# Kernel optimization log

Measured on AMD Instinct MI355X. Metric: run time of the kernel, lower is better.

Reference implementation:

```python
import jax, jax.numpy as jnp
import numpy as np

IN_BW = 4
W_BW = 4
EPS = 1e-5


def quantize(x, bw):
    # k-bit uniform quantizer on [-1, 1 - 2^(1-bw)] with straight-through rounding
    scale = 2.0 ** (bw - 1)
    xc = jnp.clip(x, -1.0, 1.0 - 1.0 / scale)
    q = jnp.round(xc * scale) / scale
    return xc + jax.lax.stop_gradient(q - xc)


def bconv(x, w, stride):
    # BinarizeConv2d: quantize activations (in_bw) and weights (weight_bw), then conv
    return jax.lax.conv_general_dilated(
        quantize(x, IN_BW), quantize(w, W_BW),
        window_strides=stride, padding='VALID',
        dimension_numbers=('NCHW', 'OIHW', 'NCHW'))


def bn2d(x, g, b):
    mean = x.mean(axis=(0, 2, 3), keepdims=True)
    var = x.var(axis=(0, 2, 3), keepdims=True)
    return (x - mean) * jax.lax.rsqrt(var + EPS) * g.reshape(1, -1, 1, 1) + b.reshape(1, -1, 1, 1)


def bn1d(x, g, b):
    mean = x.mean(axis=0, keepdims=True)
    var = x.var(axis=0, keepdims=True)
    return (x - mean) * jax.lax.rsqrt(var + EPS) * g + b


def htanh(x):
    return jnp.clip(x, -1.0, 1.0)


def setup_inputs() -> dict:
    key = jax.random.key(0)
    ks = jax.random.split(key, 24)
    B = 8192
    d = {'x': jax.random.normal(ks[0], (B, 1, 1250, 1), dtype=jnp.float32)}
    # conv weights OIHW
    shapes = [(3, 1, 6, 1), (5, 3, 5, 1), (10, 5, 4, 1), (20, 10, 4, 1), (20, 20, 4, 1)]
    for i, s in enumerate(shapes):
        d[f'w{i+1}'] = 0.3 * jax.random.normal(ks[1 + i], s, dtype=jnp.float32)
    d['fw1'] = 0.3 * jax.random.normal(ks[6], (10, 740), dtype=jnp.float32)
    d['fw2'] = 0.3 * jax.random.normal(ks[7], (2, 10), dtype=jnp.float32)
    chans = [3, 5, 10, 20, 20, 10, 2]
    for i, c in enumerate(chans):
        d[f'g{i+1}'] = 1.0 + 0.1 * jax.random.normal(ks[8 + i], (c,), dtype=jnp.float32)
        d[f'b{i+1}'] = 0.1 * jax.random.normal(ks[15 + i], (c,), dtype=jnp.float32)
    return d


def reference(x, w1, w2, w3, w4, w5, fw1, fw2,
              g1, g2, g3, g4, g5, g6, g7,
              b1, b2, b3, b4, b5, b6, b7):
    h = htanh(bn2d(bconv(x, w1, (2, 1)), g1, b1))
    h = htanh(bn2d(bconv(h, w2, (2, 1)), g2, b2))
    h = htanh(bn2d(bconv(h, w3, (2, 1)), g3, b3))
    h = htanh(bn2d(bconv(h, w4, (2, 1)), g4, b4))
    h = htanh(bn2d(bconv(h, w5, (2, 1)), g5, b5))
    h = h.reshape(h.shape[0], -1)  # (B, 20*37*1) = (B, 740)
    # dropout is identity in eval mode
    h = htanh(bn1d(quantize(h, IN_BW) @ quantize(fw1, W_BW).T, g6, b6))
    h = bn1d(quantize(h, IN_BW) @ quantize(fw2, W_BW).T, g7, b7)
    return h
```

## Files before the change

### kernel.cpp

```cpp
#include <hip/hip_runtime.h>

#define DEV __device__ __forceinline__

DEV float qwt(float w) {
    float y = fminf(fmaxf(w, -1.0f), 0.875f);
    return rintf(y * 8.0f) * 0.125f;
}
DEV int qw8i(float w) {
    float y = fminf(fmaxf(w, -1.0f), 0.875f);
    return (int)rintf(y * 8.0f);
}
DEV int q8i(float x, float a, float b) {
    float y = fmaf(x, a, b);
    y = fminf(fmaxf(y, -1.0f), 0.875f);
    return (int)rintf(y * 8.0f);
}
DEV float qact(float x, float a, float b) {
    float y = fmaf(x, a, b);
    y = fminf(fmaxf(y, -1.0f), 0.875f);
    return rintf(y * 8.0f) * 0.125f;
}

DEV int dot4(int a, int b, int c) {
#if __has_builtin(__builtin_amdgcn_sdot4)
    return __builtin_amdgcn_sdot4(a, b, c, false);
#else
    c += (int)(signed char)(a)       * (int)(signed char)(b);
    c += (int)(signed char)(a >> 8)  * (int)(signed char)(b >> 8);
    c += (int)(signed char)(a >> 16) * (int)(signed char)(b >> 16);
    c += (int)(signed char)(a >> 24) * (int)(signed char)(b >> 24);
    return c;
#endif
}
DEV unsigned alignpair(unsigned hi, unsigned lo, int bits) {
#if __has_builtin(__builtin_amdgcn_alignbit)
    return __builtin_amdgcn_alignbit(hi, lo, bits);
#else
    return bits ? ((lo >> bits) | (hi << (32 - bits))) : lo;
#endif
}

DEV void atomAddF64(double* p, double v) { atomicAdd(p, v); }

DEV void pack_layer(const float* w, int* o, int CIN, int COUT, int K, int t) {
    int KW = (K + 3) / 4;
    for (int i = t; i < COUT * CIN * KW; i += 256) {
        int j = i % KW, cc = i / KW;
        unsigned r = 0;
        for (int u = 0; u < 4; u++) {
            int k = 4 * j + u;
            int b = (k < K) ? (qw8i(w[cc * K + k]) & 0xff) : 0;
            r |= (unsigned)b << (8 * u);
        }
        o[i] = (int)r;
    }
}

template<int CIN,int COUT,int K,int LINP,int LOUT,int LOUTP,int P,int R,bool IN_FLOAT,int LIN=0>
DEV void conv_phase(
    const void* __restrict__ in_, const int* __restrict__ wqi,
    const double* __restrict__ statsIn,
    const float* __restrict__ gprev, const float* __restrict__ bprev, double Nprev,
    short* __restrict__ out, double* __restrict__ statsOut, int B, int VB,
    const float* __restrict__ wown,
    const float* __restrict__ pw2, const float* __restrict__ pw3,
    const float* __restrict__ pw4, const float* __restrict__ pw5,
    int* __restrict__ owp2, int* __restrict__ owp3,
    int* __restrict__ owp4, int* __restrict__ owp5)
{
    constexpr int KW   = (K + 3) / 4;
    constexpr int NE   = P + 2 * KW - 1;
    constexpr int ND   = (2 * (NE - 1) + 3) / 4 + 2;
    constexpr int LO_P = (LOUT + P - 1) / P;
    constexpr int GROUPS = R * LO_P;

    __shared__ __align__(16) signed char smem[R * CIN * LINP + 32];
    __shared__ float ts[CIN], tb[CIN];
    __shared__ float red[4][2 * COUT];
    __shared__ int lwq[IN_FLOAT ? (COUT * CIN * KW) : 1];

    const int tid = threadIdx.x;
    const int bid = blockIdx.x;
    const int lane = tid & 63, wid = tid >> 6;

    if constexpr (IN_FLOAT) {
        for (int i = tid; i < COUT * CIN * KW; i += 256) {
            int j = i % KW, cc = i / KW;
            unsigned rr = 0;
            for (int u = 0; u < 4; u++) {
                int k = 4 * j + u;
                int bv = (k < K) ? (qw8i(wown[cc * K + k]) & 0xff) : 0;
                rr |= (unsigned)bv << (8 * u);
            }
            lwq[i] = (int)rr;
        }
        if (bid == 0) {
            pack_layer(pw2, owp2, 3, 5, 5, tid);
            pack_layer(pw3, owp3, 5, 10, 4, tid);
            pack_layer(pw4, owp4, 10, 20, 4, tid);
            pack_layer(pw5, owp5, 20, 20, 4, tid);
        }
    } else {
        if (tid < CIN) {
            double S = 0.0, Q = 0.0;
#pragma unroll
            for (int s = 0; s < 8; s++) {
                S += statsIn[s * (2 * CIN) + 2 * tid];
                Q += statsIn[s * (2 * CIN) + 2 * tid + 1];
            }
            double mean = S / Nprev;
            double var  = Q / Nprev - mean * mean;
            double inv  = 1.0 / sqrt(var + 1e-5);
            double sc   = (double)gprev[tid] * inv;
            ts[tid] = (float)sc * 0.015625f;
            tb[tid] = (float)((double)bprev[tid] - mean * sc);
        }
    }
    __syncthreads();

    float tsum[COUT], tsq[COUT];
#pragma unroll
    for (int c = 0; c < COUT; c++) { tsum[c] = 0.f; tsq[c] = 0.f; }

#pragma unroll 1
    for (int vb = bid; vb < VB; vb += gridDim.x) {
        const int r0   = vb * R;
        const int rcnt = min(R, B - r0);

        if constexpr (IN_FLOAT) {
            constexpr int CH = LIN / 2;
            const float2* gp = (const float2*)in_;
            const int total = rcnt * CH;
#pragma unroll 1
            for (int base = 0; base < total; base += 1024) {
                float2 v[4];
#pragma unroll
                for (int u = 0; u < 4; u++) {
                    int c = base + u * 256 + tid;
                    if (c < total) v[u] = gp[(size_t)r0 * CH + c];
                }
#pragma unroll
                for (int u = 0; u < 4; u++) {
                    int c = base + u * 256 + tid;
                    if (c < total) {
                        int r = c / CH, rem = c - r * CH;
                        int b0 = q8i(v[u].x, 1.f, 0.f) & 0xff;
                        int b1 = q8i(v[u].y, 1.f, 0.f) & 0xff;
                        *(unsigned short*)(smem + r * LINP + rem * 2) =
                            (unsigned short)(b0 | (b1 << 8));
                    }
                }
            }
        } else {
            constexpr int CH  = CIN * LINP / 8;
            constexpr int CHC = LINP / 8;
            const int4* gp = (const int4*)((const short*)in_ + (size_t)r0 * CIN * LINP);
            const int total = rcnt * CH;
#pragma unroll 1
            for (int base = 0; base < total; base += 1024) {
                int4 v[4];
#pragma unroll
                for (int u = 0; u < 4; u++) {
                    int c = base + u * 256 + tid;
                    if (c < total) v[u] = gp[c];
                }
#pragma unroll
                for (int u = 0; u < 4; u++) {
                    int c = base + u * 256 + tid;
                    if (c < total) {
                        int rem = c % CH;
                        int ci = rem / CHC;
                        float a = ts[ci], bo = tb[ci];
                        int vs[4] = { v[u].x, v[u].y, v[u].z, v[u].w };
                        unsigned pk[2];
#pragma unroll
                        for (int w8 = 0; w8 < 2; w8++) {
                            unsigned pp = 0;
#pragma unroll
                            for (int j = 0; j < 2; j++) {
                                int word = vs[w8 * 2 + j];
                                int b0 = q8i((float)(short)(word & 0xffff), a, bo) & 0xff;
                                int b1 = q8i((float)(short)(word >> 16),    a, bo) & 0xff;
                                pp |= (unsigned)(b0 | (b1 << 8)) << (16 * j);
                            }
                            pk[w8] = pp;
                        }
                        ((uint2*)smem)[c] = make_uint2(pk[0], pk[1]);
                    }
                }
            }
        }
        __syncthreads();

#pragma unroll 1
        for (int g = tid; g < GROUPS; g += 256) {
            int r = g / LO_P;
            if (r >= rcnt) continue;
            int l0   = (g - r * LO_P) * P;
            int pact = min(P, LOUT - l0);

            int acc[COUT][P];
#pragma unroll
            for (int co = 0; co < COUT; co++)
#pragma unroll
                for (int p = 0; p < P; p++) acc[co][p] = 0;

            const int ibase = r * CIN * LINP + 2 * l0;
            const int sh    = (P % 2 == 0) ? 0 : (ibase & 3);

            for (int ci = 0; ci < CIN; ci++) {
                const int* sp = (const int*)smem + ((ci * LINP + (ibase & ~3)) >> 2);
                int d[ND];
#pragma unroll
                for (int j = 0; j < ND; j++) d[j] = sp[j];
                int e[NE];
#pragma unroll
                for (int i = 0; i < NE; i++) {
                    int off = sh + 2 * i;
                    e[i] = (int)alignpair((unsigned)d[off / 4 + 1], (unsigned)d[off / 4], (off & 3) * 8);
                }
#pragma unroll
                for (int co = 0; co < COUT; co++) {
#pragma unroll
                    for (int j = 0; j < KW; j++) {
                        int wv;
                        if constexpr (IN_FLOAT) wv = lwq[(co * CIN + ci) * KW + j];
                        else                    wv = wqi[(co * CIN + ci) * KW + j];
#pragma unroll
                        for (int p = 0; p < P; p++)
                            acc[co][p] = dot4(e[p + 2 * j], wv, acc[co][p]);
                    }
                }
            }

            const size_t ob = (size_t)(r0 + r) * COUT * LOUTP + l0;
#pragma unroll
            for (int co = 0; co < COUT; co++) {
                if (pact == P) {
                    short tmp[P];
#pragma unroll
                    for (int p = 0; p < P; p++) {
                        tmp[p] = (short)acc[co][p];
                        float v = (float)acc[co][p] * 0.015625f;
                        tsum[co] += v;
                        tsq[co]   = fmaf(v, v, tsq[co]);
                    }
                    short* op = &out[ob + (size_t)co * LOUTP];
                    if constexpr (P == 1) {
                        op[0] = tmp[0];
                    } else if constexpr (P == 2) {
                        *(short2*)op = make_short2(tmp[0], tmp[1]);
                    } else if constexpr (P == 4) {
                        *(short4*)op = make_short4(tmp[0], tmp[1], tmp[2], tmp[3]);
                    } else if constexpr (P == 8) {
                        *(short4*)op       = make_short4(tmp[0], tmp[1], tmp[2], tmp[3]);
                        *(short4*)(op + 4) = make_short4(tmp[4], tmp[5], tmp[6], tmp[7]);
                    }
                } else {
#pragma unroll
                    for (int p = 0; p < P; p++) {
                        if (p < pact) {
                            int k = acc[co][p];
                            out[ob + (size_t)co * LOUTP + p] = (short)k;
                            float v = (float)k * 0.015625f;
                            tsum[co] += v;
                            tsq[co]   = fmaf(v, v, tsq[co]);
                        }
                    }
                }
            }
        }
        __syncthreads();
    }

#pragma unroll
    for (int co = 0; co < COUT; co++) {
        float s = tsum[co], q = tsq[co];
        for (int off = 32; off > 0; off >>= 1) {
            s += __shfl_down(s, off, 64);
            q += __shfl_down(q, off, 64);
        }
        if (lane == 0) { red[wid][2 * co] = s; red[wid][2 * co + 1] = q; }
    }
    __syncthreads();
    if (tid < 2 * COUT) {
        float v = red[0][tid] + red[1][tid] + red[2][tid] + red[3][tid];
        atomAddF64(&statsOut[(size_t)(bid & 7) * (2 * COUT) + tid], (double)v);
    }
}

__global__ __launch_bounds__(256) void k_conv1(
    const float* x, short* y1, double* sl1, int B, int VB,
    const float* w1, const float* w2, const float* w3, const float* w4,
    const float* w5, int* wp2, int* wp3, int* wp4, int* wp5)
{
    conv_phase<1, 3, 6, 1252, 623, 624, 8, 3, true, 1250>(
        x, nullptr, nullptr, nullptr, nullptr, 0.0, y1, sl1, B, VB,
        w1, w2, w3, w4, w5, wp2, wp3, wp4, wp5);
}
__global__ __launch_bounds__(256) void k_conv2(
    const short* in_, const int* wq, const double* sIn,
    const float* g, const float* b, short* out, double* sOut, int B, int VB)
{
    conv_phase<3, 5, 5, 624, 310, 312, 4, 4, false>(
        in_, wq, sIn, g, b, 8192.0 * 623.0, out, sOut, B, VB,
        nullptr, nullptr, nullptr, nullptr, nullptr, nullptr, nullptr, nullptr, nullptr);
}
__global__ __launch_bounds__(256) void k_conv3(
    const short* in_, const int* wq, const double* sIn,
    const float* g, const float* b, short* out, double* sOut, int B, int VB)
{
    conv_phase<5, 10, 4, 312, 154, 160, 2, 4, false>(
        in_, wq, sIn, g, b, 8192.0 * 310.0, out, sOut, B, VB,
        nullptr, nullptr, nullptr, nullptr, nullptr, nullptr, nullptr, nullptr, nullptr);
}
__global__ __launch_bounds__(256) void k_conv4(
    const short* in_, const int* wq, const double* sIn,
    const float* g, const float* b, short* out, double* sOut, int B, int VB)
{
    conv_phase<10, 20, 4, 160, 76, 80, 1, 4, false>(
        in_, wq, sIn, g, b, 8192.0 * 154.0, out, sOut, B, VB,
        nullptr, nullptr, nullptr, nullptr, nullptr, nullptr, nullptr, nullptr, nullptr);
}
__global__ __launch_bounds__(256) void k_conv5(
    const short* in_, const int* wq, const double* sIn,
    const float* g, const float* b, short* out, double* sOut, int B, int VB)
{
    conv_phase<20, 20, 4, 80, 37, 40, 1, 8, false>(
        in_, wq, sIn, g, b, 8192.0 * 76.0, out, sOut, B, VB,
        nullptr, nullptr, nullptr, nullptr, nullptr, nullptr, nullptr, nullptr, nullptr);
}

__global__ __launch_bounds__(256) void k_fc1(
    const short* __restrict__ y5, const float* __restrict__ fw1,
    const double* __restrict__ statsIn,
    const float* __restrict__ g5, const float* __restrict__ b5,
    float* __restrict__ z1, double* __restrict__ statsOut, int B)
{
    __shared__ float wq[7400];
    __shared__ float ts[20], tb[20];
    __shared__ float red[4][20];

    const int tid = threadIdx.x;
    const int bid = blockIdx.x;

    for (int i = tid; i < 7400; i += 256) wq[i] = qwt(fw1[i]);
    if (tid < 20) {
        double S = 0.0, Q = 0.0;
#pragma unroll
        for (int s = 0; s < 8; s++) {
            S += statsIn[s * 40 + 2 * tid];
            Q += statsIn[s * 40 + 2 * tid + 1];
        }
        double N = 8192.0 * 37.0;
        double mean = S / N;
        double var  = Q / N - mean * mean;
        double inv  = 1.0 / sqrt(var + 1e-5);
        double sc   = (double)g5[tid] * inv;
        ts[tid] = (float)sc;
        tb[tid] = (float)((double)b5[tid] - mean * sc);
    }
    __syncthreads();

    const int lane = tid & 63, wid = tid >> 6;
    float tsum[10], tsq[10];
#pragma unroll
    for (int j = 0; j < 10; j++) { tsum[j] = 0.f; tsq[j] = 0.f; }

#pragma unroll 1
    for (int r = bid * 4 + wid; r < B; r += gridDim.x * 4) {
        const short* xr = y5 + (size_t)r * 800;
        float acc[10];
#pragma unroll
        for (int j = 0; j < 10; j++) acc[j] = 0.f;
#pragma unroll 1
        for (int f = lane; f < 740; f += 64) {
            int c = f / 37, pos = f - c * 37;
            float x = qact((float)xr[c * 40 + pos] * 0.015625f, ts[c], tb[c]);
#pragma unroll
            for (int j = 0; j < 10; j++) acc[j] = fmaf(x, wq[j * 740 + f], acc[j]);
        }
#pragma unroll
        for (int j = 0; j < 10; j++) {
            float v = acc[j];
            for (int off = 1; off < 64; off <<= 1) v += __shfl_xor(v, off, 64);
            tsum[j] += v; tsq[j] = fmaf(v, v, tsq[j]);
            if (lane == j) z1[(size_t)r * 10 + j] = v;
        }
    }
    if (lane == 0) {
#pragma unroll
        for (int j = 0; j < 10; j++) { red[wid][2 * j] = tsum[j]; red[wid][2 * j + 1] = tsq[j]; }
    }
    __syncthreads();
    if (tid < 20) {
        float v = red[0][tid] + red[1][tid] + red[2][tid] + red[3][tid];
        atomAddF64(&statsOut[(size_t)(bid & 7) * 20 + tid], (double)v);
    }
}

__global__ __launch_bounds__(256) void k_fc2(
    const float* __restrict__ z1, const float* __restrict__ fw2,
    const double* __restrict__ statsIn,
    const float* __restrict__ g6, const float* __restrict__ b6,
    const float* __restrict__ g7, const float* __restrict__ b7,
    float* __restrict__ outp, int B)
{
    __shared__ float zbuf[16384];
    __shared__ float ts7[10], tb7[10], wq2[20];
    __shared__ float fr[4][4];
    __shared__ float tr8[4];

    const int tid = threadIdx.x;
    const int lane = tid & 63, wid = tid >> 6;

    if (tid < 20) wq2[tid] = qwt(fw2[tid]);
    if (tid < 10) {
        double S = 0.0, Q = 0.0;
#pragma unroll
        for (int s = 0; s < 8; s++) {
            S += statsIn[s * 20 + 2 * tid];
            Q += statsIn[s * 20 + 2 * tid + 1];
        }
        double N = 8192.0;
        double mean = S / N;
        double var  = Q / N - mean * mean;
        double inv  = 1.0 / sqrt(var + 1e-5);
        double sc   = (double)g6[tid] * inv;
        ts7[tid] = (float)sc;
        tb7[tid] = (float)((double)b6[tid] - mean * sc);
    }
    __syncthreads();

    float s0 = 0.f, q0 = 0.f, s1 = 0.f, q1 = 0.f;
#pragma unroll 1
    for (int r = tid; r < B; r += 512) {
        const int r2 = r + 256;
        float a0 = 0.f, a1 = 0.f, c0 = 0.f, c1 = 0.f;
#pragma unroll
        for (int i = 0; i < 10; i++) {
            float xA = qact(z1[(size_t)r * 10 + i], ts7[i], tb7[i]);
            a0 = fmaf(xA, wq2[i], a0);
            a1 = fmaf(xA, wq2[10 + i], a1);
        }
#pragma unroll
        for (int i = 0; i < 10; i++) {
            float xB = qact(z1[(size_t)r2 * 10 + i], ts7[i], tb7[i]);
            c0 = fmaf(xB, wq2[i], c0);
            c1 = fmaf(xB, wq2[10 + i], c1);
        }
        zbuf[r * 2]      = a0;
        zbuf[r * 2 + 1]  = a1;
        zbuf[r2 * 2]     = c0;
        zbuf[r2 * 2 + 1] = c1;
        s0 += a0; q0 = fmaf(a0, a0, q0);
        s1 += a1; q1 = fmaf(a1, a1, q1);
        s0 += c0; q0 = fmaf(c0, c0, q0);
        s1 += c1; q1 = fmaf(c1, c1, q1);
    }
    for (int off = 32; off > 0; off >>= 1) {
        s0 += __shfl_down(s0, off, 64); q0 += __shfl_down(q0, off, 64);
        s1 += __shfl_down(s1, off, 64); q1 += __shfl_down(q1, off, 64);
    }
    if (lane == 0) { fr[wid][0] = s0; fr[wid][1] = q0; fr[wid][2] = s1; fr[wid][3] = q1; }
    __syncthreads();
    if (tid < 2) {
        double S = 0.0, Q = 0.0;
        for (int w = 0; w < 4; w++) { S += (double)fr[w][2 * tid]; Q += (double)fr[w][2 * tid + 1]; }
        double N = (double)B;
        double mean = S / N;
        double var  = Q / N - mean * mean;
        double inv  = 1.0 / sqrt(var + 1e-5);
        double sc   = (double)g7[tid] * inv;
        tr8[tid]     = (float)sc;
        tr8[2 + tid] = (float)((double)b7[tid] - mean * sc);
    }
    __syncthreads();
    for (int i = tid; i < 2 * B; i += 256) {
        int c = i & 1;
        outp[i] = fmaf(zbuf[i], tr8[c], tr8[2 + c]);
    }
}

extern "C" void kernel_launch(void* const* d_in, const int* in_sizes, int n_in,
                              void* d_out, int out_size, void* d_ws, size_t ws_size,
                              hipStream_t stream)
{
    const float* x   = (const float*)d_in[0];
    const float* w1  = (const float*)d_in[1];
    const float* w2  = (const float*)d_in[2];
    const float* w3  = (const float*)d_in[3];
    const float* w4  = (const float*)d_in[4];
    const float* w5  = (const float*)d_in[5];
    const float* fw1 = (const float*)d_in[6];
    const float* fw2 = (const float*)d_in[7];
    const float *g[7], *bb[7];
    for (int i = 0; i < 7; i++) { g[i] = (const float*)d_in[8 + 2 * i]; bb[i] = (const float*)d_in[9 + 2 * i]; }

    char* ws = (char*)d_ws;
    size_t off = 0;
    auto alloc = [&](size_t bytes) -> void* {
        void* q = ws + off;
        off += (bytes + 255) & ~(size_t)255;
        return q;
    };
    short* y1 = (short*)alloc((size_t)8192 * 3 * 624 * 2);
    short* y2 = (short*)alloc((size_t)8192 * 5 * 312 * 2);
    short* y3 = (short*)alloc((size_t)8192 * 10 * 160 * 2);
    short* y4 = (short*)alloc((size_t)8192 * 20 * 80 * 2);
    short* y5 = (short*)alloc((size_t)8192 * 20 * 40 * 2);
    float* z1 = (float*)alloc((size_t)81920 * 4);
    int*   wp2 = (int*)alloc(256);  int* wp3 = (int*)alloc(256);
    int*   wp4 = (int*)alloc(1024); int* wp5 = (int*)alloc(2048);
    double* slots = (double*)alloc((size_t)1088 * 8);
    double* sl1 = slots;
    double* sl2 = sl1 + 8 * 6;
    double* sl3 = sl2 + 8 * 10;
    double* sl4 = sl3 + 8 * 20;
    double* sl5 = sl4 + 8 * 40;
    double* sl6 = sl5 + 8 * 40;

    const int B = 8192;

    hipMemsetAsync(slots, 0, (size_t)1088 * 8, stream);

    k_conv1<<<1024, 256, 0, stream>>>(x, y1, sl1, B, 2731,
                                      w1, w2, w3, w4, w5, wp2, wp3, wp4, wp5);
    k_conv2<<<1024, 256, 0, stream>>>(y1, wp2, sl1, g[0], bb[0], y2, sl2, B, 2048);
    k_conv3<<<1024, 256, 0, stream>>>(y2, wp3, sl2, g[1], bb[1], y3, sl3, B, 2048);
    k_conv4<<<1024, 256, 0, stream>>>(y3, wp4, sl3, g[2], bb[2], y4, sl4, B, 2048);
    k_conv5<<<1024, 256, 0, stream>>>(y4, wp5, sl4, g[3], bb[3], y5, sl5, B, 1024);
    k_fc1<<<2048, 256, 0, stream>>>(y5, fw1, sl5, g[4], bb[4], z1, sl6, B);
    k_fc2<<<1, 256, 0, stream>>>(z1, fw2, sl6, g[5], bb[5], g[6], bb[6],
                                 (float*)d_out, B);
}
```

Baseline: 274.9 us.

## Use int8 dot4 packed weights for fc1 with prepacked weights

Packs the quantized fc1 weights into int8x4 words once, inside conv1's first block, instead of having every fc1 block re-quantize 7400 floats into shared memory. fc1 now quantizes activations to int8 and accumulates with sdot4 over contiguous 12-element lane chunks, with an integer wave reduction. Each wave handles exactly one row, so the grid must cover B rows exactly. The intent is to cut the per-block weight setup and the FMA work, at the cost of depending on that fixed grid size.

```diff
diff --git a/kernel.cpp b/kernel.cpp
--- a/kernel.cpp
+++ b/kernel.cpp
@@ -50,6 +50,19 @@
         for (int u = 0; u < 4; u++) {
             int k = 4 * j + u;
             int b = (k < K) ? (qw8i(w[cc * K + k]) & 0xff) : 0;
+            r |= (unsigned)b << (8 * u);
+        }
+        o[i] = (int)r;
+    }
+}
+
+DEV void pack_fc1(const float* fw1, int* o, int t) {
+    for (int i = t; i < 1920; i += 256) {
+        int j = i / 192, d = i - j * 192;
+        unsigned r = 0;
+        for (int u = 0; u < 4; u++) {
+            int f = 4 * d + u;
+            int b = (f < 740) ? (qw8i(fw1[j * 740 + f]) & 0xff) : 0;
             r |= (unsigned)b << (8 * u);
         }
         o[i] = (int)r;
@@ -292,8 +305,10 @@
 __global__ __launch_bounds__(256) void k_conv1(
     const float* x, short* y1, double* sl1, int B, int VB,
     const float* w1, const float* w2, const float* w3, const float* w4,
-    const float* w5, int* wp2, int* wp3, int* wp4, int* wp5)
-{
+    const float* w5, int* wp2, int* wp3, int* wp4, int* wp5,
+    const float* fw1, int* wp6)
+{
+    if (blockIdx.x == 0) pack_fc1(fw1, wp6, threadIdx.x);
     conv_phase<1, 3, 6, 1252, 623, 624, 8, 3, true, 1250>(
         x, nullptr, nullptr, nullptr, nullptr, 0.0, y1, sl1, B, VB,
         w1, w2, w3, w4, w5, wp2, wp3, wp4, wp5);
@@ -332,19 +347,20 @@
 }
 
 __global__ __launch_bounds__(256) void k_fc1(
-    const short* __restrict__ y5, const float* __restrict__ fw1,
+    const short* __restrict__ y5, const int* __restrict__ wp6,
     const double* __restrict__ statsIn,
     const float* __restrict__ g5, const float* __restrict__ b5,
     float* __restrict__ z1, double* __restrict__ statsOut, int B)
 {
-    __shared__ float wq[7400];
+    __shared__ int wqi[1920];
     __shared__ float ts[20], tb[20];
     __shared__ float red[4][20];
 
     const int tid = threadIdx.x;
     const int bid = blockIdx.x;
-
-    for (int i = tid; i < 7400; i += 256) wq[i] = qwt(fw1[i]);
+    const int lane = tid & 63, wid = tid >> 6;
+
+    for (int i = tid; i < 1920; i += 256) wqi[i] = wp6[i];
     if (tid < 20) {
         double S = 0.0, Q = 0.0;
 #pragma unroll
@@ -362,31 +378,44 @@
     }
     __syncthreads();
 
-    const int lane = tid & 63, wid = tid >> 6;
+    const int r = bid * 4 + wid;
+    const short* xr = y5 + (size_t)r * 800;
+    const int f0 = lane * 12;
+
+    int q[12];
+#pragma unroll
+    for (int u = 0; u < 12; u++) {
+        int f = f0 + u;
+        int val = 0;
+        if (f < 740) {
+            int c = f / 37, pos = f - c * 37;
+            val = q8i((float)xr[c * 40 + pos] * 0.015625f, ts[c], tb[c]);
+        }
+        q[u] = val & 0xff;
+    }
+    int xp[3];
+#pragma unroll
+    for (int d = 0; d < 3; d++)
+        xp[d] = q[4 * d] | (q[4 * d + 1] << 8) | (q[4 * d + 2] << 16) | (q[4 * d + 3] << 24);
+
+    int ia[10];
+#pragma unroll
+    for (int j = 0; j < 10; j++) {
+        int a = 0;
+#pragma unroll
+        for (int d = 0; d < 3; d++)
+            a = dot4(xp[d], wqi[j * 192 + lane * 3 + d], a);
+        ia[j] = a;
+    }
+
     float tsum[10], tsq[10];
 #pragma unroll
-    for (int j = 0; j < 10; j++) { tsum[j] = 0.f; tsq[j] = 0.f; }
-
-#pragma unroll 1
-    for (int r = bid * 4 + wid; r < B; r += gridDim.x * 4) {
-        const short* xr = y5 + (size_t)r * 800;
-        float acc[10];
-#pragma unroll
-        for (int j = 0; j < 10; j++) acc[j] = 0.f;
-#pragma unroll 1
-        for (int f = lane; f < 740; f += 64) {
-            int c = f / 37, pos = f - c * 37;
-            float x = qact((float)xr[c * 40 + pos] * 0.015625f, ts[c], tb[c]);
-#pragma unroll
-            for (int j = 0; j < 10; j++) acc[j] = fmaf(x, wq[j * 740 + f], acc[j]);
-        }
-#pragma unroll
-        for (int j = 0; j < 10; j++) {
-            float v = acc[j];
-            for (int off = 1; off < 64; off <<= 1) v += __shfl_xor(v, off, 64);
-            tsum[j] += v; tsq[j] = fmaf(v, v, tsq[j]);
-            if (lane == j) z1[(size_t)r * 10 + j] = v;
-        }
+    for (int j = 0; j < 10; j++) {
+        int a = ia[j];
+        for (int off = 1; off < 64; off <<= 1) a += __shfl_xor(a, off, 64);
+        float v = (float)a * 0.015625f;
+        tsum[j] = v; tsq[j] = v * v;
+        if (lane == j) z1[(size_t)r * 10 + j] = v;
     }
     if (lane == 0) {
 #pragma unroll
@@ -512,6 +541,7 @@
     float* z1 = (float*)alloc((size_t)81920 * 4);
     int*   wp2 = (int*)alloc(256);  int* wp3 = (int*)alloc(256);
     int*   wp4 = (int*)alloc(1024); int* wp5 = (int*)alloc(2048);
+    int*   wp6 = (int*)alloc(7680);
     double* slots = (double*)alloc((size_t)1088 * 8);
     double* sl1 = slots;
     double* sl2 = sl1 + 8 * 6;
@@ -525,12 +555,13 @@
     hipMemsetAsync(slots, 0, (size_t)1088 * 8, stream);
 
     k_conv1<<<1024, 256, 0, stream>>>(x, y1, sl1, B, 2731,
-                                      w1, w2, w3, w4, w5, wp2, wp3, wp4, wp5);
+                                      w1, w2, w3, w4, w5, wp2, wp3, wp4, wp5,
+                                      fw1, wp6);
     k_conv2<<<1024, 256, 0, stream>>>(y1, wp2, sl1, g[0], bb[0], y2, sl2, B, 2048);
     k_conv3<<<1024, 256, 0, stream>>>(y2, wp3, sl2, g[1], bb[1], y3, sl3, B, 2048);
     k_conv4<<<1024, 256, 0, stream>>>(y3, wp4, sl3, g[2], bb[2], y4, sl4, B, 2048);
     k_conv5<<<1024, 256, 0, stream>>>(y4, wp5, sl4, g[3], bb[3], y5, sl5, B, 1024);
-    k_fc1<<<2048, 256, 0, stream>>>(y5, fw1, sl5, g[4], bb[4], z1, sl6, B);
+    k_fc1<<<2048, 256, 0, stream>>>(y5, wp6, sl5, g[4], bb[4], z1, sl6, B);
     k_fc2<<<1, 256, 0, stream>>>(z1, fw2, sl6, g[5], bb[5], g[6], bb[6],
                                  (float*)d_out, B);
 }
```

Result: no change. 273.9 us (-0.4%).
